# Kernel optimization log

Measured on AMD Instinct MI355X. Metric: run time of the kernel, lower is better.

The kernel has to match this reference:

```python
import jax, jax.numpy as jnp
import numpy as np

B, N_RX, IMG_H, IMG_W = 128, 34, 512, 512
N_CAT = 5  # num_rx_categories + 1


def setup_inputs() -> dict:
    key = jax.random.key(0)
    k_pow, k_xy, k_cat, k_dw, k_db, k_cw, k_cb = jax.random.split(key, 7)
    # x_vecs columns: [power, x_coord, y_coord, category]
    powers = jax.random.normal(k_pow, (B, N_RX, 1), dtype=jnp.float32)
    coords = jax.random.randint(k_xy, (B, N_RX, 2), 0, IMG_W).astype(jnp.float32)
    cats = jax.random.randint(k_cat, (B, N_RX, 1), 0, N_CAT).astype(jnp.float32)
    x_vecs = jnp.concatenate([powers, coords, cats], axis=-1)  # [B, N_RX, 4]
    # learned per-device and per-category affine parameters (init: ones/zeros,
    # perturbed slightly so the test is non-trivial)
    device_weights = 1.0 + 0.1 * jax.random.normal(k_dw, (N_RX,), dtype=jnp.float32)
    device_bias = 0.1 * jax.random.normal(k_db, (N_RX,), dtype=jnp.float32)
    category_weights = 1.0 + 0.1 * jax.random.normal(k_cw, (N_CAT,), dtype=jnp.float32)
    category_bias = 0.1 * jax.random.normal(k_cb, (N_CAT,), dtype=jnp.float32)
    return {
        "x_vecs": x_vecs,
        "device_weights": device_weights,
        "device_bias": device_bias,
        "category_weights": category_weights,
        "category_bias": category_bias,
    }


def reference(x_vecs, device_weights, device_bias, category_weights, category_bias):
    batch, n_rx = x_vecs.shape[0], x_vecs.shape[1]
    raw_powers = x_vecs[:, :, 0]                      # [B, N]
    power_mask = (raw_powers != 0).astype(x_vecs.dtype)
    # per-device affine (device_multiplication)
    p = raw_powers * device_weights + power_mask * device_bias
    # per-category affine (category_multiplication)
    cat = x_vecs[:, :, -1].astype(jnp.int32)          # [B, N]
    p = p * category_weights[cat] + power_mask * category_bias[cat]
    # coordinate-based scatter into image grid
    coords = jnp.round(x_vecs[:, :, 1:3]).astype(jnp.int32)  # [B, N, 2] (x, y)
    b_idx = jnp.repeat(jnp.arange(batch), n_rx)
    yy = coords[:, :, 1].ravel()
    xx = coords[:, :, 0].ravel()
    x_img = jnp.zeros((batch, 2, IMG_H, IMG_W), dtype=x_vecs.dtype)
    x_img = x_img.at[b_idx, 0, yy, xx].set(p.ravel())
    x_img = x_img.at[b_idx, 1, yy, xx].set(raw_powers.ravel())
    return x_img
```

## Files before the change

kernel.cpp:

```cpp
#include <hip/hip_runtime.h>

#define B_BATCH 128
#define N_RX 34
#define IMG 512
#define PLANE (IMG * IMG)
#define REGION (2 * PLANE)
#define THREADS 256
#define FLOATS_PER_THREAD 16
#define FLOATS_PER_BLOCK (THREADS * FLOATS_PER_THREAD)
#define BLOCKS_PER_BATCH (REGION / FLOATS_PER_BLOCK)
#define N_ENT (2 * N_RX)

typedef float vfloat4 __attribute__((ext_vector_type(4)));

__global__ __launch_bounds__(THREADS)
void Vec2Im_fused_kernel(const float4* __restrict__ xv,
                         const float* __restrict__ dw,
                         const float* __restrict__ db,
                         const float* __restrict__ cw,
                         const float* __restrict__ cb,
                         float* __restrict__ out) {
    __shared__ int   s_pos[N_ENT];
    __shared__ float s_val[N_ENT];
    __shared__ int   s_fpos[N_ENT];
    __shared__ float s_fval[N_ENT];
    __shared__ int   s_cnt;

    const int b     = blockIdx.x >> 7;
    const int chunk = blockIdx.x & (BLOCKS_PER_BATCH - 1);
    const int t     = threadIdx.x;

    if (t < N_RX) {
        float4 v = xv[(size_t)b * N_RX + t];
        float raw  = v.x;
        float mask = (raw != 0.0f) ? 1.0f : 0.0f;
        float p = raw * dw[t] + mask * db[t];
        int cat = (int)v.w;
        p = p * cw[cat] + mask * cb[cat];
        int xx = (int)rintf(v.y);
        int yy = (int)rintf(v.z);
        int off = yy * IMG + xx;
        s_pos[t]        = off;               s_val[t]        = p;
        s_pos[N_RX + t] = off + PLANE;       s_val[N_RX + t] = raw;
    }
    __syncthreads();

    if (t == 0) {
        const int lo = chunk * FLOATS_PER_BLOCK;
        const int hi = lo + FLOATS_PER_BLOCK;
        int c = 0;
        for (int i = 0; i < N_ENT; ++i) {
            int p = s_pos[i];
            if (p >= lo && p < hi) { s_fpos[c] = p - lo; s_fval[c] = s_val[i]; ++c; }
        }
        s_cnt = c;
    }
    __syncthreads();

    vfloat4 v0 = {0.f, 0.f, 0.f, 0.f};
    vfloat4 v1 = {0.f, 0.f, 0.f, 0.f};
    vfloat4 v2 = {0.f, 0.f, 0.f, 0.f};
    vfloat4 v3 = {0.f, 0.f, 0.f, 0.f};

    const int cnt = s_cnt;
    for (int i = 0; i < cnt; ++i) {
        int q  = s_fpos[i];
        int f  = q >> 2;
        bool mine = ((f & (THREADS - 1)) == t);
        float vv  = s_fval[i];
        int k  = f >> 8;
        int e  = q & 3;
        if (mine && k == 0) { if (e==0) v0.x=vv; else if (e==1) v0.y=vv; else if (e==2) v0.z=vv; else v0.w=vv; }
        if (mine && k == 1) { if (e==0) v1.x=vv; else if (e==1) v1.y=vv; else if (e==2) v1.z=vv; else v1.w=vv; }
        if (mine && k == 2) { if (e==0) v2.x=vv; else if (e==1) v2.y=vv; else if (e==2) v2.z=vv; else v2.w=vv; }
        if (mine && k == 3) { if (e==0) v3.x=vv; else if (e==1) v3.y=vv; else if (e==2) v3.z=vv; else v3.w=vv; }
    }

    vfloat4* o4 = (vfloat4*)(out + (size_t)b * REGION + (size_t)chunk * FLOATS_PER_BLOCK);
    __builtin_nontemporal_store(v0, o4 + t);
    __builtin_nontemporal_store(v1, o4 + THREADS + t);
    __builtin_nontemporal_store(v2, o4 + 2 * THREADS + t);
    __builtin_nontemporal_store(v3, o4 + 3 * THREADS + t);
}

extern "C" void kernel_launch(void* const* d_in, const int* in_sizes, int n_in,
                              void* d_out, int out_size, void* d_ws, size_t ws_size,
                              hipStream_t stream) {
    const float4* x_vecs          = (const float4*)d_in[0];
    const float* device_weights   = (const float*)d_in[1];
    const float* device_bias      = (const float*)d_in[2];
    const float* category_weights = (const float*)d_in[3];
    const float* category_bias    = (const float*)d_in[4];
    float* out = (float*)d_out;

    Vec2Im_fused_kernel<<<B_BATCH * BLOCKS_PER_BATCH, THREADS, 0, stream>>>(
        x_vecs, device_weights, device_bias, category_weights, category_bias, out);
}
```

Measured before the change: 288.6 us.

## Split per-batch affine prep into separate kernel and enlarge fill tiles

Moves the per-receiver affine and coordinate computation into a small prep kernel that writes positions and values to workspace, so fill blocks no longer recompute them. Fill blocks now each cover 16 float4 per thread (four times larger), cutting block count, and write zeros with nontemporal stores followed by scalar scatter of the few nonzero entries by one thread. This adds an extra kernel launch and a dependency through workspace, and relies on store ordering within a block after a barrier for the scatter to overwrite the zeros.

```diff
diff --git a/kernel.cpp b/kernel.cpp
--- a/kernel.cpp
+++ b/kernel.cpp
@@ -6,81 +6,83 @@
 #define PLANE (IMG * IMG)
 #define REGION (2 * PLANE)
 #define THREADS 256
-#define FLOATS_PER_THREAD 16
-#define FLOATS_PER_BLOCK (THREADS * FLOATS_PER_THREAD)
+#define F4_PER_THREAD 16
+#define FLOATS_PER_BLOCK (THREADS * F4_PER_THREAD * 4)
 #define BLOCKS_PER_BATCH (REGION / FLOATS_PER_BLOCK)
 #define N_ENT (2 * N_RX)
 
 typedef float vfloat4 __attribute__((ext_vector_type(4)));
 
+__global__ __launch_bounds__(64)
+void Vec2Im_prep_kernel(const float4* __restrict__ xv,
+                        const float* __restrict__ dw,
+                        const float* __restrict__ db,
+                        const float* __restrict__ cw,
+                        const float* __restrict__ cb,
+                        int* __restrict__ pos, float* __restrict__ val) {
+    const int b = blockIdx.x;
+    const int t = threadIdx.x;
+    if (t >= N_RX) return;
+    float4 v = xv[(size_t)b * N_RX + t];
+    float raw  = v.x;
+    float mask = (raw != 0.0f) ? 1.0f : 0.0f;
+    float p = raw * dw[t] + mask * db[t];
+    int cat = (int)v.w;
+    p = p * cw[cat] + mask * cb[cat];
+    int xx = (int)rintf(v.y);
+    int yy = (int)rintf(v.z);
+    int off = yy * IMG + xx;
+    pos[b * N_ENT + t]        = off;           val[b * N_ENT + t]        = p;
+    pos[b * N_ENT + N_RX + t] = off + PLANE;   val[b * N_ENT + N_RX + t] = raw;
+}
+
 __global__ __launch_bounds__(THREADS)
-void Vec2Im_fused_kernel(const float4* __restrict__ xv,
-                         const float* __restrict__ dw,
-                         const float* __restrict__ db,
-                         const float* __restrict__ cw,
-                         const float* __restrict__ cb,
-                         float* __restrict__ out) {
+void Vec2Im_fill_kernel(const int* __restrict__ pos,
+                        const float* __restrict__ val,
+                        float* __restrict__ out) {
     __shared__ int   s_pos[N_ENT];
     __shared__ float s_val[N_ENT];
-    __shared__ int   s_fpos[N_ENT];
-    __shared__ float s_fval[N_ENT];
+    __shared__ int   s_fq[N_ENT];
+    __shared__ float s_fv[N_ENT];
     __shared__ int   s_cnt;
 
-    const int b     = blockIdx.x >> 7;
-    const int chunk = blockIdx.x & (BLOCKS_PER_BATCH - 1);
+    const int b     = blockIdx.x / BLOCKS_PER_BATCH;
+    const int chunk = blockIdx.x % BLOCKS_PER_BATCH;
     const int t     = threadIdx.x;
 
-    if (t < N_RX) {
-        float4 v = xv[(size_t)b * N_RX + t];
-        float raw  = v.x;
-        float mask = (raw != 0.0f) ? 1.0f : 0.0f;
-        float p = raw * dw[t] + mask * db[t];
-        int cat = (int)v.w;
-        p = p * cw[cat] + mask * cb[cat];
-        int xx = (int)rintf(v.y);
-        int yy = (int)rintf(v.z);
-        int off = yy * IMG + xx;
-        s_pos[t]        = off;               s_val[t]        = p;
-        s_pos[N_RX + t] = off + PLANE;       s_val[N_RX + t] = raw;
+    if (t < N_ENT) {
+        s_pos[t] = pos[b * N_ENT + t];
+        s_val[t] = val[b * N_ENT + t];
     }
     __syncthreads();
 
     if (t == 0) {
         const int lo = chunk * FLOATS_PER_BLOCK;
-        const int hi = lo + FLOATS_PER_BLOCK;
         int c = 0;
         for (int i = 0; i < N_ENT; ++i) {
-            int p = s_pos[i];
-            if (p >= lo && p < hi) { s_fpos[c] = p - lo; s_fval[c] = s_val[i]; ++c; }
+            int q = s_pos[i] - lo;
+            if ((unsigned)q < (unsigned)FLOATS_PER_BLOCK) {
+                s_fq[c] = q; s_fv[c] = s_val[i]; ++c;
+            }
         }
         s_cnt = c;
     }
     __syncthreads();
 
-    vfloat4 v0 = {0.f, 0.f, 0.f, 0.f};
-    vfloat4 v1 = {0.f, 0.f, 0.f, 0.f};
-    vfloat4 v2 = {0.f, 0.f, 0.f, 0.f};
-    vfloat4 v3 = {0.f, 0.f, 0.f, 0.f};
+    float* base = out + (size_t)b * REGION + (size_t)chunk * FLOATS_PER_BLOCK;
+    vfloat4* o4 = (vfloat4*)base;
+    const vfloat4 z = {0.f, 0.f, 0.f, 0.f};
+#pragma unroll
+    for (int k = 0; k < F4_PER_THREAD; ++k)
+        __builtin_nontemporal_store(z, o4 + k * THREADS + t);
 
-    const int cnt = s_cnt;
-    for (int i = 0; i < cnt; ++i) {
-        int q  = s_fpos[i];
-        int f  = q >> 2;
-        bool mine = ((f & (THREADS - 1)) == t);
-        float vv  = s_fval[i];
-        int k  = f >> 8;
-        int e  = q & 3;
-        if (mine && k == 0) { if (e==0) v0.x=vv; else if (e==1) v0.y=vv; else if (e==2) v0.z=vv; else v0.w=vv; }
-        if (mine && k == 1) { if (e==0) v1.x=vv; else if (e==1) v1.y=vv; else if (e==2) v1.z=vv; else v1.w=vv; }
-        if (mine && k == 2) { if (e==0) v2.x=vv; else if (e==1) v2.y=vv; else if (e==2) v2.z=vv; else v2.w=vv; }
-        if (mine && k == 3) { if (e==0) v3.x=vv; else if (e==1) v3.y=vv; else if (e==2) v3.z=vv; else v3.w=vv; }
+    if (s_cnt != 0) {
+        __syncthreads();
+        if (t == 0) {
+            const int c = s_cnt;
+            for (int i = 0; i < c; ++i) base[s_fq[i]] = s_fv[i];
+        }
     }
-
-    vfloat4* o4 = (vfloat4*)(out + (size_t)b * REGION + (size_t)chunk * FLOATS_PER_BLOCK);
-    __builtin_nontemporal_store(v0, o4 + t);
-    __builtin_nontemporal_store(v1, o4 + THREADS + t);
-    __builtin_nontemporal_store(v2, o4 + 2 * THREADS + t);
-    __builtin_nontemporal_store(v3, o4 + 3 * THREADS + t);
 }
 
 extern "C" void kernel_launch(void* const* d_in, const int* in_sizes, int n_in,
@@ -93,6 +95,13 @@
     const float* category_bias    = (const float*)d_in[4];
     float* out = (float*)d_out;
 
-    Vec2Im_fused_kernel<<<B_BATCH * BLOCKS_PER_BATCH, THREADS, 0, stream>>>(
-        x_vecs, device_weights, device_bias, category_weights, category_bias, out);
+    int*   ws_pos = (int*)d_ws;
+    float* ws_val = (float*)((char*)d_ws + B_BATCH * N_ENT * sizeof(int));
+
+    Vec2Im_prep_kernel<<<B_BATCH, 64, 0, stream>>>(
+        x_vecs, device_weights, device_bias, category_weights, category_bias,
+        ws_pos, ws_val);
+
+    Vec2Im_fill_kernel<<<B_BATCH * BLOCKS_PER_BATCH, THREADS, 0, stream>>>(
+        ws_pos, ws_val, out);
 }
```

Result: faster. 281.1 us (-2.6%).
